# Optimization experiments

Hardware: AMD Instinct MI355X
Metric: run time of the kernel (lower is better)

Reference implementation:

```python
import jax, jax.numpy as jnp
import numpy as np
import math

B, S, HID, H = 8, 512, 768, 12
D = HID // H  # 64
LABEL_VOCAB = 2 * 40 + 1  # 81
EPS = 1e-5


def layernorm(x, g, b):
    mu = jnp.mean(x, axis=-1, keepdims=True)
    var = jnp.var(x, axis=-1, keepdims=True)
    return (x - mu) * jax.lax.rsqrt(var + EPS) * g + b


def setup_inputs() -> dict:
    key = jax.random.key(0)
    ks = jax.random.split(key, 12)
    s = 0.02
    return {
        "hidden_states": jax.random.normal(ks[0], (B, S, HID), jnp.float32),
        "attention_mask": jnp.zeros((B, 1, 1, S), jnp.float32),
        "graph_arc": jax.random.randint(ks[1], (B, S, S), 0, LABEL_VOCAB, jnp.int32),
        "Wq": jax.random.normal(ks[2], (HID, HID), jnp.float32) * s,
        "bq": jnp.zeros((HID,), jnp.float32),
        "Wk": jax.random.normal(ks[3], (HID, HID), jnp.float32) * s,
        "bk": jnp.zeros((HID,), jnp.float32),
        "Wv": jax.random.normal(ks[4], (HID, HID), jnp.float32) * s,
        "bv": jnp.zeros((HID,), jnp.float32),
        "rel_k": jax.random.normal(ks[5], (LABEL_VOCAB, D), jnp.float32) * s,
        "rel_v": jax.random.normal(ks[6], (LABEL_VOCAB, D), jnp.float32) * s,
        "ln_k_g": jnp.ones((D,), jnp.float32),
        "ln_k_b": jnp.zeros((D,), jnp.float32),
        "ln_v_g": jnp.ones((D,), jnp.float32),
        "ln_v_b": jnp.zeros((D,), jnp.float32),
    }


def reference(hidden_states, attention_mask, graph_arc, Wq, bq, Wk, bk, Wv, bv,
              rel_k, rel_v, ln_k_g, ln_k_b, ln_v_g, ln_v_b):
    # projections -> [B, H, S, D]
    def split_heads(x):
        return x.reshape(B, S, H, D).transpose(0, 2, 1, 3)

    q = split_heads(hidden_states @ Wq + bq)
    k = split_heads(hidden_states @ Wk + bk)
    v = split_heads(hidden_states @ Wv + bv)

    # relation embeddings [B, S, S, D], layernormed over D
    dp_keys = layernorm(rel_k[graph_arc], ln_k_g, ln_k_b)
    dp_values = layernorm(rel_v[graph_arc], ln_v_g, ln_v_b)

    scores = jnp.einsum('bhqd,bhkd->bhqk', q, k) / math.sqrt(D)
    # relative_matmul_dp: per (b, q-position) GEMM of q[B,S,H,D] with dp_keys^T
    scores = scores + jnp.einsum('bqhd,bqkd->bhqk', q.transpose(0, 2, 1, 3), dp_keys)
    scores = scores + attention_mask

    probs = jax.nn.softmax(scores, axis=-1)  # dropout p=0 (eval)

    ctx = jnp.einsum('bhqk,bhkd->bqhd', probs, v)
    # relative_matmul_dpv
    ctx = ctx + jnp.einsum('bhqk,bqkd->bqhd', probs, dp_values)
    return ctx.reshape(B, S, HID)
```

## Files before the change

kernel.cpp:

```cpp
#include <hip/hip_runtime.h>
#include <hip/hip_bf16.h>

#define BB 8
#define SS 512
#define HIDV 768
#define HH 12
#define DD 64
#define LV 81

typedef __attribute__((ext_vector_type(8))) short short8v;
typedef __attribute__((ext_vector_type(4))) short short4v;
typedef __attribute__((ext_vector_type(4))) float f32x4;

#define MFMA16(a, b, c) __builtin_amdgcn_mfma_f32_16x16x32_bf16(a, b, c, 0, 0, 0)

__device__ __forceinline__ short f2bf(float f) {
    __hip_bfloat16 h = __float2bfloat16(f);
    return *reinterpret_cast<short*>(&h);
}
__device__ __forceinline__ float bf2f(short s) {
    __hip_bfloat16 h = *reinterpret_cast<__hip_bfloat16*>(&s);
    return __bfloat162float(h);
}
__device__ __forceinline__ void gload16(const void* g, void* l) {
    __builtin_amdgcn_global_load_lds((const __attribute__((address_space(1))) void*)g,
                                     (__attribute__((address_space(3))) void*)l, 16, 0, 0);
}

__global__ __launch_bounds__(256) void prep_ln_kernel(
    const float* __restrict__ rel_k, const float* __restrict__ rel_v,
    const float* __restrict__ gk, const float* __restrict__ bk,
    const float* __restrict__ gv, const float* __restrict__ bv,
    short* __restrict__ lnkb, short* __restrict__ lnvT) {
    __shared__ float ln_lds[2 * LV][DD];
    int t = threadIdx.x;
    if (t < 2 * LV) {
        bool isv = (t >= LV);
        int r = isv ? t - LV : t;
        const float* row = (isv ? rel_v : rel_k) + r * DD;
        const float* g = isv ? gv : gk;
        const float* be = isv ? bv : bk;
        float mu = 0.f;
        for (int d = 0; d < DD; ++d) mu += row[d];
        mu *= (1.f / DD);
        float var = 0.f;
        for (int d = 0; d < DD; ++d) { float x = row[d] - mu; var += x * x; }
        var *= (1.f / DD);
        float rs = rsqrtf(var + 1e-5f);
        for (int d = 0; d < DD; ++d) ln_lds[t][d] = (row[d] - mu) * rs * g[d] + be[d];
    }
    __syncthreads();
    for (int i = t; i < 96 * DD; i += 256) {
        int l = i >> 6, d = i & 63;
        lnkb[i] = (l < LV) ? f2bf(ln_lds[l][d]) : (short)0;
    }
    for (int i = t; i < DD * 96; i += 256) {
        int d = i / 96, ll = i - d * 96;
        lnvT[i] = (ll < LV) ? f2bf(ln_lds[LV + ll][d]) : (short)0;
    }
}

__global__ __launch_bounds__(256) void conv_hidden_kernel(const float* __restrict__ in,
                                                          short* __restrict__ out) {
    int i = (blockIdx.x * 256 + threadIdx.x) * 4;
    float4 v = *reinterpret_cast<const float4*>(&in[i]);
    short4v o; o[0] = f2bf(v.x); o[1] = f2bf(v.y); o[2] = f2bf(v.z); o[3] = f2bf(v.w);
    *reinterpret_cast<short4v*>(&out[i]) = o;
}

__global__ __launch_bounds__(256) void transw_kernel(
    const float* __restrict__ Wq, const float* __restrict__ Wk, const float* __restrict__ Wv,
    short* __restrict__ WqT, short* __restrict__ WkT, short* __restrict__ WvT) {
    const float* W; short* O;
    if (blockIdx.z == 0) { W = Wq; O = WqT; }
    else if (blockIdx.z == 1) { W = Wk; O = WkT; }
    else { W = Wv; O = WvT; }
    __shared__ float tile[32][33];
    int k0 = blockIdx.y * 32, n0 = blockIdx.x * 32;
    int t = threadIdx.x;
    int r = t >> 3, c4 = (t & 7) * 4;
    float4 v = *reinterpret_cast<const float4*>(&W[(size_t)(k0 + r) * HIDV + n0 + c4]);
    tile[r][c4 + 0] = v.x; tile[r][c4 + 1] = v.y; tile[r][c4 + 2] = v.z; tile[r][c4 + 3] = v.w;
    __syncthreads();
    short4v o;
    o[0] = f2bf(tile[c4 + 0][r]); o[1] = f2bf(tile[c4 + 1][r]);
    o[2] = f2bf(tile[c4 + 2][r]); o[3] = f2bf(tile[c4 + 3][r]);
    *reinterpret_cast<short4v*>(&O[(size_t)(n0 + r) * HIDV + k0 + c4]) = o;
}

__global__ __launch_bounds__(256) void arcpack_kernel(const int* __restrict__ arc,
                                                      unsigned int* __restrict__ arcP) {
    __shared__ unsigned int tbuf[64][129];
    const int tid = threadIdx.x;
    const int b = blockIdx.y;
    const int q0 = blockIdx.x * 64;
    for (int i = tid; i < 64 * 128; i += 256) {
        int r = i >> 7, c4 = i & 127;
        int4 v = *reinterpret_cast<const int4*>(&arc[((size_t)(b * SS) + q0 + r) * SS + 4 * c4]);
        tbuf[r][c4] = (unsigned)(v.x & 255) | ((unsigned)(v.y & 255) << 8) |
                      ((unsigned)(v.z & 255) << 16) | ((unsigned)(v.w & 255) << 24);
    }
    __syncthreads();
    for (int i = tid; i < 128 * 64; i += 256) {
        int k4 = i >> 6, r = i & 63;
        arcP[((size_t)b * 128 + k4) * SS + q0 + r] = tbuf[r][k4];
    }
}

__global__ __launch_bounds__(256) void qkv_gemm_kernel(
    const short* __restrict__ Abf,
    const short* __restrict__ WqT, const short* __restrict__ WkT, const short* __restrict__ WvT,
    const float* __restrict__ bq, const float* __restrict__ bk, const float* __restrict__ bv,
    short* __restrict__ qo, short* __restrict__ ko, short* __restrict__ vto) {
    const short* Bt; const float* bias;
    int z = blockIdx.z;
    if (z == 0) { Bt = WqT; bias = bq; }
    else if (z == 1) { Bt = WkT; bias = bk; }
    else { Bt = WvT; bias = bv; }

    __shared__ short smem[8192];
    short* As = smem;
    short* Bs = smem + 4096;

    const int tid = threadIdx.x;
    const int lane = tid & 63, w = tid >> 6;
    const int li = lane & 15, g = lane >> 4;
    const int wr = w >> 1, wc = w & 1;
    const int m0 = blockIdx.y * 64, n0 = blockIdx.x * 64;

    f32x4 acc[2][2];
    for (int ra = 0; ra < 2; ++ra)
        for (int cb = 0; cb < 2; ++cb)
            for (int r = 0; r < 4; ++r) acc[ra][cb][r] = 0.f;

#pragma unroll 1
    for (int k0 = 0; k0 < HIDV; k0 += 64) {
#pragma unroll
        for (int j = 0; j < 2; ++j) {
            int c = j * 256 + tid;
            int row = c >> 3, s = c & 7;
            int src = s ^ (row & 7);
            gload16(Abf + (size_t)(m0 + row) * HIDV + k0 + src * 8, As + c * 8);
            gload16(Bt + (size_t)(n0 + row) * HIDV + k0 + src * 8, Bs + c * 8);
        }
        __syncthreads();
#pragma unroll
        for (int c = 0; c < 2; ++c) {
            short8v af[2], bf[2];
#pragma unroll
            for (int ra = 0; ra < 2; ++ra) {
                int row = 32 * wr + 16 * ra + li;
                int chunk = (4 * c + g) ^ (row & 7);
                af[ra] = *reinterpret_cast<const short8v*>(&As[row * 64 + chunk * 8]);
            }
#pragma unroll
            for (int cb = 0; cb < 2; ++cb) {
                int rowb = 32 * wc + 16 * cb + li;
                int chunk = (4 * c + g) ^ (rowb & 7);
                bf[cb] = *reinterpret_cast<const short8v*>(&Bs[rowb * 64 + chunk * 8]);
            }
#pragma unroll
            for (int ra = 0; ra < 2; ++ra)
#pragma unroll
                for (int cb = 0; cb < 2; ++cb)
                    acc[ra][cb] = MFMA16(af[ra], bf[cb], acc[ra][cb]);
        }
        __syncthreads();
    }

    const int h = n0 >> 6;
    const int bidx = m0 >> 9;
    if (z < 2) {
        short* dst = (z == 0) ? qo : ko;
        float sc = (z == 0) ? 1.f : 0.125f;
#pragma unroll
        for (int ra = 0; ra < 2; ++ra)
#pragma unroll
            for (int cb = 0; cb < 2; ++cb) {
                int n = 32 * wc + 16 * cb + li;
                float bv_ = bias[n0 + n];
#pragma unroll
                for (int r = 0; r < 4; ++r) {
                    int m = m0 + 32 * wr + 16 * ra + 4 * g + r;
                    int s = m & 511;
                    dst[(((size_t)bidx * HH + h) * SS + s) * DD + n] =
                        f2bf((acc[ra][cb][r] + bv_) * sc);
                }
            }
    } else {
        short* Cs = smem;
#pragma unroll
        for (int ra = 0; ra < 2; ++ra)
#pragma unroll
            for (int cb = 0; cb < 2; ++cb) {
                int nl = 32 * wc + 16 * cb + li;
                float bv_ = bias[n0 + nl];
#pragma unroll
                for (int r = 0; r < 4; ++r) {
                    int ml = 32 * wr + 16 * ra + 4 * g + r;
                    Cs[nl * 72 + ml] = f2bf(acc[ra][cb][r] + bv_);
                }
            }
        __syncthreads();
        for (int c = tid; c < 512; c += 256) {
            int dl = c >> 3, s8 = (c & 7) * 8;
            short8v vv = *reinterpret_cast<const short8v*>(&Cs[dl * 72 + s8]);
            *reinterpret_cast<short8v*>(
                &vto[(((size_t)bidx * HH + h) * DD + dl) * SS + (m0 & 511) + s8]) = vv;
        }
    }
}

__global__ __launch_bounds__(256, 3) void attn_kernel(
    const short* __restrict__ qb, const short* __restrict__ kb, const short* __restrict__ vt,
    const unsigned int* __restrict__ arcP, const float* __restrict__ maskp,
    const short* __restrict__ lnkb, const short* __restrict__ lnvT,
    float* __restrict__ outp) {
    __shared__ float qlds[4][16][84];
    __shared__ float bucket[4][16][96];

    const int tid = threadIdx.x;
    const int w = tid >> 6, lane = tid & 63;
    const int li = lane & 15, g = lane >> 4;
    const int bx = blockIdx.x;
    const int b = bx & 7;
    const int rest = bx >> 3;
    const int h = rest % HH, qt = rest / HH;
    const int bh = b * HH + h;
    const int q0 = qt * 64 + w * 16;

    const short* kbp = kb + (size_t)bh * SS * DD;
    const short* vbp = vt + (size_t)bh * DD * SS;

    for (int i = lane; i < 16 * 96; i += 64) (&bucket[w][0][0])[i] = 0.f;

    short8v qf[2];
    {
        const short* qrow = qb + ((size_t)bh * SS + q0 + li) * DD + 8 * g;
        qf[0] = *reinterpret_cast<const short8v*>(qrow);
        qf[1] = *reinterpret_cast<const short8v*>(qrow + 32);
    }

    {
        f32x4 qr[6];
#pragma unroll
        for (int ct = 0; ct < 6; ++ct) {
            f32x4 a = {0.f, 0.f, 0.f, 0.f};
            short8v b0 = *reinterpret_cast<const short8v*>(&lnkb[(16 * ct + li) * DD + 8 * g]);
            short8v b1 = *reinterpret_cast<const short8v*>(&lnkb[(16 * ct + li) * DD + 32 + 8 * g]);
            a = MFMA16(qf[0], b0, a);
            a = MFMA16(qf[1], b1, a);
            qr[ct] = a;
        }
#pragma unroll
        for (int ct = 0; ct < 6; ++ct)
#pragma unroll
            for (int r = 0; r < 4; ++r)
                if (16 * ct + li < 84) qlds[w][4 * g + r][16 * ct + li] = qr[ct][r];
    }

    f32x4 oacc[4];
    for (int t = 0; t < 4; ++t) for (int r = 0; r < 4; ++r) oacc[t][r] = 0.f;
    float lsum = 0.f;

#pragma unroll 2
    for (int kt = 0; kt < 8; ++kt) {
        const int kb0 = kt * 64;

        unsigned int a4[4];
#pragma unroll
        for (int t = 0; t < 4; ++t)
            a4[t] = arcP[((size_t)b * 128 + kt * 16 + 4 * t + g) * SS + q0 + li];

        float4 mv[4];
#pragma unroll
        for (int t = 0; t < 4; ++t)
            mv[t] = *reinterpret_cast<const float4*>(&maskp[(size_t)b * SS + kb0 + 16 * t + 4 * g]);

        f32x4 sacc[4];
#pragma unroll
        for (int t = 0; t < 4; ++t) {
            const short* kr = kbp + (size_t)(kb0 + 16 * t + li) * DD + 8 * g;
            short8v k0 = *reinterpret_cast<const short8v*>(kr);
            short8v k1 = *reinterpret_cast<const short8v*>(kr + 32);
            f32x4 a = {0.f, 0.f, 0.f, 0.f};
            a = MFMA16(k0, qf[0], a);
            a = MFMA16(k1, qf[1], a);
            sacc[t] = a;
        }

        short8v pfrag[2];
#pragma unroll
        for (int t = 0; t < 4; ++t) {
            float pv[4];
#pragma unroll
            for (int r = 0; r < 4; ++r) {
                const int a_ = (a4[t] >> (8 * r)) & 255;
                float s = sacc[t][r] + qlds[w][li][a_] +
                          reinterpret_cast<const float*>(&mv[t])[r];
                float p = __expf(s);
                lsum += p;
                atomicAdd(&bucket[w][li][a_], p);
                pv[r] = p;
            }
#pragma unroll
            for (int r = 0; r < 4; ++r) pfrag[t >> 1][4 * (t & 1) + r] = f2bf(pv[r]);
        }

#pragma unroll
        for (int dt = 0; dt < 2; ++dt) {
#pragma unroll
            for (int t2 = 0; t2 < 4; ++t2) {
                const short* vr = vbp + (size_t)(16 * t2 + li) * SS + kb0 + 32 * dt + 4 * g;
                short4v v0 = *reinterpret_cast<const short4v*>(vr);
                short4v v1 = *reinterpret_cast<const short4v*>(vr + 16);
                short8v vf;
                vf[0] = v0[0]; vf[1] = v0[1]; vf[2] = v0[2]; vf[3] = v0[3];
                vf[4] = v1[0]; vf[5] = v1[1]; vf[6] = v1[2]; vf[7] = v1[3];
                oacc[t2] = MFMA16(pfrag[dt], vf, oacc[t2]);
            }
        }
    }

    lsum += __shfl_xor(lsum, 16);
    lsum += __shfl_xor(lsum, 32);
    float inv = 1.f / lsum;
    float invr[4];
#pragma unroll
    for (int r = 0; r < 4; ++r) invr[r] = __shfl(inv, 4 * g + r);

    f32x4 racc[4];
    for (int t = 0; t < 4; ++t) for (int r = 0; r < 4; ++r) racc[t][r] = 0.f;
#pragma unroll
    for (int c = 0; c < 3; ++c) {
        f32x4 b0 = *reinterpret_cast<const f32x4*>(&bucket[w][li][8 * g + 32 * c]);
        f32x4 b1 = *reinterpret_cast<const f32x4*>(&bucket[w][li][8 * g + 32 * c + 4]);
        short8v bfr;
        bfr[0] = f2bf(b0[0]); bfr[1] = f2bf(b0[1]); bfr[2] = f2bf(b0[2]); bfr[3] = f2bf(b0[3]);
        bfr[4] = f2bf(b1[0]); bfr[5] = f2bf(b1[1]); bfr[6] = f2bf(b1[2]); bfr[7] = f2bf(b1[3]);
#pragma unroll
        for (int t2 = 0; t2 < 4; ++t2) {
            short8v lf = *reinterpret_cast<const short8v*>(
                &lnvT[(16 * t2 + li) * 96 + 8 * g + 32 * c]);
            racc[t2] = MFMA16(bfr, lf, racc[t2]);
        }
    }

#pragma unroll
    for (int t2 = 0; t2 < 4; ++t2)
#pragma unroll
        for (int r = 0; r < 4; ++r) {
            int row = q0 + 4 * g + r;
            outp[((size_t)b * SS + row) * HIDV + h * DD + 16 * t2 + li] =
                (oacc[t2][r] + racc[t2][r]) * invr[r];
        }
}

extern "C" void kernel_launch(void* const* d_in, const int* in_sizes, int n_in,
                              void* d_out, int out_size, void* d_ws, size_t ws_size,
                              hipStream_t stream) {
    const float* hidden = (const float*)d_in[0];
    const float* mask   = (const float*)d_in[1];
    const int*   arc    = (const int*)d_in[2];
    const float* Wq = (const float*)d_in[3];
    const float* bq = (const float*)d_in[4];
    const float* Wk = (const float*)d_in[5];
    const float* bk = (const float*)d_in[6];
    const float* Wv = (const float*)d_in[7];
    const float* bv = (const float*)d_in[8];
    const float* rel_k = (const float*)d_in[9];
    const float* rel_v = (const float*)d_in[10];
    const float* lng_k = (const float*)d_in[11];
    const float* lnb_k = (const float*)d_in[12];
    const float* lng_v = (const float*)d_in[13];
    const float* lnb_v = (const float*)d_in[14];
    float* out = (float*)d_out;

    char* p = (char*)d_ws;
    auto carve = [&](size_t bytes) { char* r = p; p += (bytes + 255) & ~(size_t)255; return r; };
    short* lnkb = (short*)carve((size_t)96 * DD * 2);
    short* lnvT = (short*)carve((size_t)DD * 96 * 2);
    short* hbf  = (short*)carve((size_t)BB * SS * HIDV * 2);
    short* WqT  = (short*)carve((size_t)HIDV * HIDV * 2);
    short* WkT  = (short*)carve((size_t)HIDV * HIDV * 2);
    short* WvT  = (short*)carve((size_t)HIDV * HIDV * 2);
    const size_t per = (size_t)BB * HH * SS * DD;
    short* qbuf = (short*)carve(per * 2);
    short* kbuf = (short*)carve(per * 2);
    short* vtb  = (short*)carve(per * 2);
    unsigned int* arcP = (unsigned int*)carve((size_t)BB * 128 * SS * 4);

    prep_ln_kernel<<<1, 256, 0, stream>>>(rel_k, rel_v, lng_k, lnb_k, lng_v, lnb_v, lnkb, lnvT);
    conv_hidden_kernel<<<(BB * SS * HIDV) / 1024, 256, 0, stream>>>(hidden, hbf);
    transw_kernel<<<dim3(24, 24, 3), 256, 0, stream>>>(Wq, Wk, Wv, WqT, WkT, WvT);
    arcpack_kernel<<<dim3(8, BB), 256, 0, stream>>>(arc, arcP);
    qkv_gemm_kernel<<<dim3(HIDV / 64, (BB * SS) / 64, 3), 256, 0, stream>>>(
        hbf, WqT, WkT, WvT, bq, bk, bv, qbuf, kbuf, vtb);
    attn_kernel<<<dim3(BB * HH * 8), 256, 0, stream>>>(
        qbuf, kbuf, vtb, arcP, mask, lnkb, lnvT, out);
}
```

Baseline: 199.0 us.

## Software-pipeline K/arc/mask loads and derive row sums from LDS buckets

Fully unrolls the key loop and double-buffers the K fragments, arc indices and mask values, so loads for the next tile are issued while the current tile's MFMAs and exponentials run. The softmax denominator is no longer accumulated per element; it is computed afterwards by summing the per-label LDS bucket histogram. Atomic adds become unsafeAtomicAdd, the bucket row stride is padded to 100 to reduce bank conflicts, and occupancy is lowered from 3 to 2 waves per SIMD to leave room for the larger register footprint. The risk is lower latency hiding from reduced occupancy, and a small numeric change because the row sum now comes from atomically accumulated buckets.

```diff
diff --git a/kernel.cpp b/kernel.cpp
--- a/kernel.cpp
+++ b/kernel.cpp
@@ -17,10 +17,6 @@
 __device__ __forceinline__ short f2bf(float f) {
     __hip_bfloat16 h = __float2bfloat16(f);
     return *reinterpret_cast<short*>(&h);
-}
-__device__ __forceinline__ float bf2f(short s) {
-    __hip_bfloat16 h = *reinterpret_cast<__hip_bfloat16*>(&s);
-    return __bfloat162float(h);
 }
 __device__ __forceinline__ void gload16(const void* g, void* l) {
     __builtin_amdgcn_global_load_lds((const __attribute__((address_space(1))) void*)g,
@@ -211,13 +207,13 @@
     }
 }
 
-__global__ __launch_bounds__(256, 3) void attn_kernel(
+__global__ __launch_bounds__(256, 2) void attn_kernel(
     const short* __restrict__ qb, const short* __restrict__ kb, const short* __restrict__ vt,
     const unsigned int* __restrict__ arcP, const float* __restrict__ maskp,
     const short* __restrict__ lnkb, const short* __restrict__ lnvT,
     float* __restrict__ outp) {
     __shared__ float qlds[4][16][84];
-    __shared__ float bucket[4][16][96];
+    __shared__ float bucket[4][16][100];
 
     const int tid = threadIdx.x;
     const int w = tid >> 6, lane = tid & 63;
@@ -231,82 +227,98 @@
 
     const short* kbp = kb + (size_t)bh * SS * DD;
     const short* vbp = vt + (size_t)bh * DD * SS;
-
-    for (int i = lane; i < 16 * 96; i += 64) (&bucket[w][0][0])[i] = 0.f;
-
-    short8v qf[2];
+    const unsigned int* apb = arcP + (size_t)b * 128 * SS;
+    const float* mkb = maskp + (size_t)b * SS;
+
+    for (int i = lane; i < 16 * 100; i += 64) (&bucket[w][0][0])[i] = 0.f;
+
+    short8v qf0, qf1;
     {
         const short* qrow = qb + ((size_t)bh * SS + q0 + li) * DD + 8 * g;
-        qf[0] = *reinterpret_cast<const short8v*>(qrow);
-        qf[1] = *reinterpret_cast<const short8v*>(qrow + 32);
-    }
-
-    {
-        f32x4 qr[6];
-#pragma unroll
-        for (int ct = 0; ct < 6; ++ct) {
-            f32x4 a = {0.f, 0.f, 0.f, 0.f};
-            short8v b0 = *reinterpret_cast<const short8v*>(&lnkb[(16 * ct + li) * DD + 8 * g]);
-            short8v b1 = *reinterpret_cast<const short8v*>(&lnkb[(16 * ct + li) * DD + 32 + 8 * g]);
-            a = MFMA16(qf[0], b0, a);
-            a = MFMA16(qf[1], b1, a);
-            qr[ct] = a;
-        }
-#pragma unroll
-        for (int ct = 0; ct < 6; ++ct)
-#pragma unroll
-            for (int r = 0; r < 4; ++r)
-                if (16 * ct + li < 84) qlds[w][4 * g + r][16 * ct + li] = qr[ct][r];
+        qf0 = *reinterpret_cast<const short8v*>(qrow);
+        qf1 = *reinterpret_cast<const short8v*>(qrow + 32);
+    }
+
+#pragma unroll
+    for (int ct = 0; ct < 6; ++ct) {
+        f32x4 a = {0.f, 0.f, 0.f, 0.f};
+        short8v b0 = *reinterpret_cast<const short8v*>(&lnkb[(16 * ct + li) * DD + 8 * g]);
+        short8v b1 = *reinterpret_cast<const short8v*>(&lnkb[(16 * ct + li) * DD + 32 + 8 * g]);
+        a = MFMA16(qf0, b0, a);
+        a = MFMA16(qf1, b1, a);
+        if (16 * ct + li < 84)
+#pragma unroll
+            for (int r = 0; r < 4; ++r) qlds[w][4 * g + r][16 * ct + li] = a[r];
     }
 
     f32x4 oacc[4];
     for (int t = 0; t < 4; ++t) for (int r = 0; r < 4; ++r) oacc[t][r] = 0.f;
-    float lsum = 0.f;
-
-#pragma unroll 2
+
+    short8v kf[8];
+    unsigned int a_[2][4];
+    float4 m_[2][4];
+#pragma unroll
+    for (int t = 0; t < 4; ++t) {
+        const short* kr = kbp + (size_t)(16 * t + li) * DD + 8 * g;
+        kf[2 * t] = *reinterpret_cast<const short8v*>(kr);
+        kf[2 * t + 1] = *reinterpret_cast<const short8v*>(kr + 32);
+        a_[0][t] = apb[(size_t)(4 * t + g) * SS + q0 + li];
+        m_[0][t] = *reinterpret_cast<const float4*>(&mkb[16 * t + 4 * g]);
+    }
+
+#pragma unroll
     for (int kt = 0; kt < 8; ++kt) {
+        const int cur = kt & 1, nxt = cur ^ 1;
         const int kb0 = kt * 64;
 
-        unsigned int a4[4];
+        f32x4 sacc[4];
+#pragma unroll
+        for (int t = 0; t < 4; ++t) {
+            f32x4 a = {0.f, 0.f, 0.f, 0.f};
+            a = MFMA16(kf[2 * t], qf0, a);
+            a = MFMA16(kf[2 * t + 1], qf1, a);
+            sacc[t] = a;
+        }
+
+        if (kt < 7) {
+#pragma unroll
+            for (int t = 0; t < 4; ++t) {
+                const short* kr = kbp + (size_t)(kb0 + 64 + 16 * t + li) * DD + 8 * g;
+                kf[2 * t] = *reinterpret_cast<const short8v*>(kr);
+                kf[2 * t + 1] = *reinterpret_cast<const short8v*>(kr + 32);
+                a_[nxt][t] = apb[(size_t)((kt + 1) * 16 + 4 * t + g) * SS + q0 + li];
+                m_[nxt][t] = *reinterpret_cast<const float4*>(&mkb[kb0 + 64 + 16 * t + 4 * g]);
+            }
+        }
+
+        float p[16];
+#pragma unroll
+        for (int t = 0; t < 4; ++t) {
+            const unsigned int a4 = a_[cur][t];
+            float qv0 = qlds[w][li][a4 & 255];
+            float qv1 = qlds[w][li][(a4 >> 8) & 255];
+            float qv2 = qlds[w][li][(a4 >> 16) & 255];
+            float qv3 = qlds[w][li][a4 >> 24];
+            p[4 * t + 0] = __expf(sacc[t][0] + qv0 + m_[cur][t].x);
+            p[4 * t + 1] = __expf(sacc[t][1] + qv1 + m_[cur][t].y);
+            p[4 * t + 2] = __expf(sacc[t][2] + qv2 + m_[cur][t].z);
+            p[4 * t + 3] = __expf(sacc[t][3] + qv3 + m_[cur][t].w);
+        }
+
+#pragma unroll
+        for (int t = 0; t < 4; ++t) {
+            const unsigned int a4 = a_[cur][t];
+            unsafeAtomicAdd(&bucket[w][li][a4 & 255], p[4 * t + 0]);
+            unsafeAtomicAdd(&bucket[w][li][(a4 >> 8) & 255], p[4 * t + 1]);
+            unsafeAtomicAdd(&bucket[w][li][(a4 >> 16) & 255], p[4 * t + 2]);
+            unsafeAtomicAdd(&bucket[w][li][a4 >> 24], p[4 * t + 3]);
+        }
+
+        short8v pfrag[2];
 #pragma unroll
         for (int t = 0; t < 4; ++t)
-            a4[t] = arcP[((size_t)b * 128 + kt * 16 + 4 * t + g) * SS + q0 + li];
-
-        float4 mv[4];
-#pragma unroll
-        for (int t = 0; t < 4; ++t)
-            mv[t] = *reinterpret_cast<const float4*>(&maskp[(size_t)b * SS + kb0 + 16 * t + 4 * g]);
-
-        f32x4 sacc[4];
-#pragma unroll
-        for (int t = 0; t < 4; ++t) {
-            const short* kr = kbp + (size_t)(kb0 + 16 * t + li) * DD + 8 * g;
-            short8v k0 = *reinterpret_cast<const short8v*>(kr);
-            short8v k1 = *reinterpret_cast<const short8v*>(kr + 32);
-            f32x4 a = {0.f, 0.f, 0.f, 0.f};
-            a = MFMA16(k0, qf[0], a);
-            a = MFMA16(k1, qf[1], a);
-            sacc[t] = a;
-        }
-
-        short8v pfrag[2];
-#pragma unroll
-        for (int t = 0; t < 4; ++t) {
-            float pv[4];
-#pragma unroll
-            for (int r = 0; r < 4; ++r) {
-                const int a_ = (a4[t] >> (8 * r)) & 255;
-                float s = sacc[t][r] + qlds[w][li][a_] +
-                          reinterpret_cast<const float*>(&mv[t])[r];
-                float p = __expf(s);
-                lsum += p;
-                atomicAdd(&bucket[w][li][a_], p);
-                pv[r] = p;
-            }
-#pragma unroll
-            for (int r = 0; r < 4; ++r) pfrag[t >> 1][4 * (t & 1) + r] = f2bf(pv[r]);
-        }
-
+#pragma unroll
+            for (int r = 0; r < 4; ++r) pfrag[t >> 1][4 * (t & 1) + r] = f2bf(p[4 * t + r]);
 #pragma unroll
         for (int dt = 0; dt < 2; ++dt) {
 #pragma unroll
@@ -322,6 +334,12 @@
         }
     }
 
+    float lsum = 0.f;
+#pragma unroll
+    for (int j = 0; j < 24; ++j) {
+        int c = 24 * g + j;
+        lsum += (c < 81) ? bucket[w][li][c] : 0.f;
+    }
     lsum += __shfl_xor(lsum, 16);
     lsum += __shfl_xor(lsum, 32);
     float inv = 1.f / lsum;
```

After: 196.0 us. No clear change (-1.6%).
